# Kernel optimization log

Hardware: AMD Instinct MI355X
Metric: run time of the kernel (lower is better)

## Reference

```python
import jax, jax.numpy as jnp
import numpy as np

D_MODEL = 1024
NUM_HEADS = 16
HEAD_DIM = D_MODEL // NUM_HEADS
HIDDEN = 4096
EPS = 1e-5


def setup_inputs() -> dict:
    key = jax.random.key(0)
    ks = jax.random.split(key, 10)
    s = 0.02
    return {
        "x": jax.random.normal(ks[0], (2, 2048, D_MODEL), dtype=jnp.float32),
        # attention projection weights stored as (in, out): y = x @ W
        "wq": jax.random.normal(ks[1], (D_MODEL, D_MODEL), dtype=jnp.float32) * s,
        "wk": jax.random.normal(ks[2], (D_MODEL, D_MODEL), dtype=jnp.float32) * s,
        "wv": jax.random.normal(ks[3], (D_MODEL, D_MODEL), dtype=jnp.float32) * s,
        "wo": jax.random.normal(ks[4], (D_MODEL, D_MODEL), dtype=jnp.float32) * s,
        # FFN
        "w1": jax.random.normal(ks[5], (D_MODEL, HIDDEN), dtype=jnp.float32) * s,
        "b1": jnp.zeros((HIDDEN,), dtype=jnp.float32),
        "w2": jax.random.normal(ks[6], (HIDDEN, D_MODEL), dtype=jnp.float32) * s,
        "b2": jnp.zeros((D_MODEL,), dtype=jnp.float32),
        # LayerNorms
        "g1": jnp.ones((D_MODEL,), dtype=jnp.float32),
        "be1": jnp.zeros((D_MODEL,), dtype=jnp.float32),
        "g2": jnp.ones((D_MODEL,), dtype=jnp.float32),
        "be2": jnp.zeros((D_MODEL,), dtype=jnp.float32),
    }


def _layernorm(x, g, b):
    mu = jnp.mean(x, axis=-1, keepdims=True)
    var = jnp.mean(jnp.square(x - mu), axis=-1, keepdims=True)
    return (x - mu) * jax.lax.rsqrt(var + EPS) * g + b


def _attention(x, wq, wk, wv, wo):
    B, S, D = x.shape
    q = (x @ wq).reshape(B, S, NUM_HEADS, HEAD_DIM)
    k = (x @ wk).reshape(B, S, NUM_HEADS, HEAD_DIM)
    v = (x @ wv).reshape(B, S, NUM_HEADS, HEAD_DIM)
    scores = jnp.einsum("bqhd,bkhd->bhqk", q, k) / jnp.sqrt(
        jnp.float32(HEAD_DIM)
    )
    causal = jnp.tril(jnp.ones((S, S), dtype=bool))
    scores = jnp.where(causal, scores, -jnp.inf)
    probs = jax.nn.softmax(scores, axis=-1)
    out = jnp.einsum("bhqk,bkhd->bqhd", probs, v).reshape(B, S, D)
    return out @ wo


def _ffn(x, w1, b1, w2, b2):
    return jax.nn.relu(x @ w1 + b1) @ w2 + b2


def reference(x, wq, wk, wv, wo, w1, b1, w2, b2, g1, be1, g2, be2):
    x = x + _attention(_layernorm(x, g1, be1), wq, wk, wv, wo)
    x = x + _ffn(_layernorm(x, g2, be2), w1, b1, w2, b2)
    return x
```

## Files before the change

kernel.cpp:

```cpp
#include <hip/hip_runtime.h>
#include <stdint.h>

typedef unsigned short bf16u;
typedef __attribute__((ext_vector_type(8))) __bf16 bf16x8;
typedef __attribute__((ext_vector_type(4))) float f32x4;
typedef __attribute__((ext_vector_type(4))) unsigned short u16x4;

typedef __attribute__((address_space(1))) void gvoid_t;
typedef __attribute__((address_space(3))) void lvoid_t;

#define SEQ 2048
#define DM 1024

__device__ __forceinline__ bf16u f2bf(float f) {
  union { float f; uint32_t u; } v; v.f = f;
  uint32_t u = v.u + 0x7fffu + ((v.u >> 16) & 1u);
  return (bf16u)(u >> 16);
}

__device__ __forceinline__ void async_copy16(const bf16u* g, const bf16u* l) {
  __builtin_amdgcn_global_load_lds((gvoid_t*)(uintptr_t)g,
                                   (lvoid_t*)(uint32_t)(uintptr_t)l,
                                   16, 0, 0);
}

__global__ __launch_bounds__(256) void ln_kernel(const float* __restrict__ x,
                                                 const float* __restrict__ g,
                                                 const float* __restrict__ be,
                                                 bf16u* __restrict__ out) {
  const int row = blockIdx.x;
  const int t = threadIdx.x;
  const float4 v = ((const float4*)(x + (size_t)row * DM))[t];
  float s  = v.x + v.y + v.z + v.w;
  float ss = v.x * v.x + v.y * v.y + v.z * v.z + v.w * v.w;
#pragma unroll
  for (int m = 1; m < 64; m <<= 1) {
    s  += __shfl_xor(s, m, 64);
    ss += __shfl_xor(ss, m, 64);
  }
  __shared__ float red[2][4];
  const int wv = t >> 6, ln = t & 63;
  if (ln == 0) { red[0][wv] = s; red[1][wv] = ss; }
  __syncthreads();
  s  = red[0][0] + red[0][1] + red[0][2] + red[0][3];
  ss = red[1][0] + red[1][1] + red[1][2] + red[1][3];
  const float mu = s * (1.0f / DM);
  const float var = ss * (1.0f / DM) - mu * mu;
  const float rstd = rsqrtf(var + 1e-5f);
  const float4 gg = ((const float4*)g)[t];
  const float4 bb = ((const float4*)be)[t];
  u16x4 o;
  o[0] = f2bf((v.x - mu) * rstd * gg.x + bb.x);
  o[1] = f2bf((v.y - mu) * rstd * gg.y + bb.y);
  o[2] = f2bf((v.z - mu) * rstd * gg.z + bb.z);
  o[3] = f2bf((v.w - mu) * rstd * gg.w + bb.w);
  *(u16x4*)(out + (size_t)row * DM + t * 4) = o;
}

__global__ __launch_bounds__(256) void wtrans(const float* __restrict__ in,
                                              bf16u* __restrict__ out, int R, int C) {
  __shared__ float tile[32][33];
  const int c0 = blockIdx.x * 32, r0 = blockIdx.y * 32;
  const int tx = threadIdx.x, ty = threadIdx.y;
#pragma unroll
  for (int i = 0; i < 4; ++i)
    tile[ty + i * 8][tx] = in[(size_t)(r0 + ty + i * 8) * C + c0 + tx];
  __syncthreads();
#pragma unroll
  for (int i = 0; i < 4; ++i)
    out[(size_t)(c0 + ty + i * 8) * R + r0 + tx] = f2bf(tile[tx][ty + i * 8]);
}

__global__ __launch_bounds__(256) void wtrans4(const float* __restrict__ a,
                                               const float* __restrict__ b,
                                               const float* __restrict__ c,
                                               const float* __restrict__ d,
                                               bf16u* __restrict__ out) {
  const float* srcs[4] = {a, b, c, d};
  const float* in = srcs[blockIdx.z];
  bf16u* o = out + (size_t)blockIdx.z * 1024 * 1024;
  __shared__ float tile[32][33];
  const int c0 = blockIdx.x * 32, r0 = blockIdx.y * 32;
  const int tx = threadIdx.x, ty = threadIdx.y;
#pragma unroll
  for (int i = 0; i < 4; ++i)
    tile[ty + i * 8][tx] = in[(size_t)(r0 + ty + i * 8) * 1024 + c0 + tx];
  __syncthreads();
#pragma unroll
  for (int i = 0; i < 4; ++i)
    o[(size_t)(c0 + ty + i * 8) * 1024 + r0 + tx] = f2bf(tile[tx][ty + i * 8]);
}

__global__ __launch_bounds__(256) void vtrans(const bf16u* __restrict__ qkv,
                                              bf16u* __restrict__ vt) {
  __shared__ bf16u tile[32][33];
  const int s0 = blockIdx.x * 32;
  const int d0 = blockIdx.y * 32;
  const int bh = blockIdx.z, b = bh >> 4, h = bh & 15;
  const int tx = threadIdx.x, ty = threadIdx.y;
#pragma unroll
  for (int i = 0; i < 4; ++i)
    tile[ty + i * 8][tx] =
        qkv[(size_t)(b * SEQ + s0 + ty + i * 8) * 3072 + 2048 + h * 64 + d0 + tx];
  __syncthreads();
#pragma unroll
  for (int i = 0; i < 4; ++i)
    vt[(size_t)(bh * 64 + d0 + ty + i * 8) * SEQ + s0 + tx] = tile[tx][ty + i * 8];
}

#define VM_WAIT(n) asm volatile("s_waitcnt vmcnt(" #n ")" ::: "memory")
#define BARRIER()  asm volatile("s_barrier" ::: "memory")

__global__ __launch_bounds__(256, 3) void gemm_bt(
    const bf16u* __restrict__ A, const bf16u* __restrict__ Bt,
    int M, int N, int K,
    const float* __restrict__ bias, const float* __restrict__ resid,
    bf16u* __restrict__ outB, float* __restrict__ outF, int mode) {
  __shared__ bf16u As0[128 * 32], As1[128 * 32];
  __shared__ bf16u Bs0[128 * 32], Bs1[128 * 32];
  const int t = threadIdx.x;
  const int wv = t >> 6, ln = t & 63;
  const int col16 = ln & 15, quad = ln >> 4;
  const int wm = wv & 1, wn = wv >> 1;
  const int m0 = blockIdx.y * 128, n0 = blockIdx.x * 128;

  const int c0 = t, c1 = 256 + t;
  const bf16u* ga0 = A + (size_t)(m0 + (c0 >> 2)) * K + (c0 & 3) * 8;
  const bf16u* ga1 = A + (size_t)(m0 + (c1 >> 2)) * K + (c1 & 3) * 8;
  const bf16u* gb0 = Bt + (size_t)(n0 + (c0 >> 2)) * K + (c0 & 3) * 8;
  const bf16u* gb1 = Bt + (size_t)(n0 + (c1 >> 2)) * K + (c1 & 3) * 8;

  const int aoff = (wm * 64 + col16) * 32 + quad * 8;
  const int boff = (wn * 64 + col16) * 32 + quad * 8;

  f32x4 acc[4][4] = {};

  auto stage = [&](bf16u* dA, bf16u* dB) {
    async_copy16(ga0, dA + (size_t)c0 * 8);
    async_copy16(ga1, dA + (size_t)c1 * 8);
    async_copy16(gb0, dB + (size_t)c0 * 8);
    async_copy16(gb1, dB + (size_t)c1 * 8);
    ga0 += 32; ga1 += 32; gb0 += 32; gb1 += 32;
  };
  auto compute = [&](const bf16u* sA, const bf16u* sB) {
    bf16x8 af[4], bfv[4];
#pragma unroll
    for (int i = 0; i < 4; ++i) af[i] = *(const bf16x8*)(sA + aoff + i * 512);
#pragma unroll
    for (int i = 0; i < 4; ++i) bfv[i] = *(const bf16x8*)(sB + boff + i * 512);
#pragma unroll
    for (int mi = 0; mi < 4; ++mi)
#pragma unroll
      for (int ni = 0; ni < 4; ++ni)
        acc[mi][ni] = __builtin_amdgcn_mfma_f32_16x16x32_bf16(af[mi], bfv[ni],
                                                              acc[mi][ni], 0, 0, 0);
  };

  const int niter = K >> 5;
  stage(As0, Bs0);
  for (int k = 0; k < niter; k += 2) {
    stage(As1, Bs1);
    VM_WAIT(4);
    BARRIER();
    compute(As0, Bs0);
    BARRIER();
    if (k + 2 < niter) {
      stage(As0, Bs0);
      VM_WAIT(4);
    } else {
      VM_WAIT(0);
    }
    BARRIER();
    compute(As1, Bs1);
    BARRIER();
  }

#pragma unroll
  for (int mi = 0; mi < 4; ++mi) {
#pragma unroll
    for (int ni = 0; ni < 4; ++ni) {
      const int col = n0 + wn * 64 + ni * 16 + col16;
#pragma unroll
      for (int r = 0; r < 4; ++r) {
        const int row = m0 + wm * 64 + mi * 16 + quad * 4 + r;
        float v = acc[mi][ni][r];
        if (mode == 1 || mode == 3) v += bias[col];
        if (mode == 1) v = fmaxf(v, 0.0f);
        if (mode >= 2) {
          outF[(size_t)row * N + col] = v + resid[(size_t)row * N + col];
        } else {
          outB[(size_t)row * N + col] = f2bf(v);
        }
      }
    }
  }
}

__global__ __launch_bounds__(256, 3) void gemm_bt64(
    const bf16u* __restrict__ A, const bf16u* __restrict__ Bt,
    int M, int N, int K,
    const float* __restrict__ bias, const float* __restrict__ resid,
    bf16u* __restrict__ outB, float* __restrict__ outF, int mode) {
  __shared__ bf16u As0[64 * 64], As1[64 * 64];
  __shared__ bf16u Bs0[128 * 64], Bs1[128 * 64];
  const int t = threadIdx.x;
  const int ln = t & 63;
  const int wv = t >> 6;
  const int col16 = ln & 15, quad = ln >> 4;
  const int m0 = blockIdx.y * 64, n0 = blockIdx.x * 128;

  const bf16u* gA[2];
  const bf16u* gB[4];
#pragma unroll
  for (int j = 0; j < 2; ++j) {
    const int c = t + 256 * j, row = c >> 3, slot = (c & 7) ^ (row & 7);
    gA[j] = A + (size_t)(m0 + row) * K + slot * 8;
  }
#pragma unroll
  for (int j = 0; j < 4; ++j) {
    const int c = t + 256 * j, row = c >> 3, slot = (c & 7) ^ (row & 7);
    gB[j] = Bt + (size_t)(n0 + row) * K + slot * 8;
  }

  f32x4 acc[4][2] = {};

  auto stage = [&](bf16u* dA, bf16u* dB) {
#pragma unroll
    for (int j = 0; j < 2; ++j) {
      async_copy16(gA[j], dA + (size_t)(t + 256 * j) * 8);
      gA[j] += 64;
    }
#pragma unroll
    for (int j = 0; j < 4; ++j) {
      async_copy16(gB[j], dB + (size_t)(t + 256 * j) * 8);
      gB[j] += 64;
    }
  };
  auto compute = [&](const bf16u* sA, const bf16u* sB) {
    bf16x8 af[4][2], bfv[2][2];
#pragma unroll
    for (int mi = 0; mi < 4; ++mi) {
      const int row = mi * 16 + col16;
#pragma unroll
      for (int kc = 0; kc < 2; ++kc)
        af[mi][kc] = *(const bf16x8*)(sA + row * 64 + (((kc << 2) + quad) ^ (row & 7)) * 8);
    }
#pragma unroll
    for (int ni = 0; ni < 2; ++ni) {
      const int row = wv * 32 + ni * 16 + col16;
#pragma unroll
      for (int kc = 0; kc < 2; ++kc)
        bfv[ni][kc] = *(const bf16x8*)(sB + row * 64 + (((kc << 2) + quad) ^ (row & 7)) * 8);
    }
#pragma unroll
    for (int kc = 0; kc < 2; ++kc)
#pragma unroll
      for (int mi = 0; mi < 4; ++mi)
#pragma unroll
        for (int ni = 0; ni < 2; ++ni)
          acc[mi][ni] = __builtin_amdgcn_mfma_f32_16x16x32_bf16(af[mi][kc], bfv[ni][kc],
                                                                acc[mi][ni], 0, 0, 0);
  };

  const int niter = K >> 6;
  stage(As0, Bs0);
  for (int k = 0; k < niter; k += 2) {
    stage(As1, Bs1);
    VM_WAIT(6);
    BARRIER();
    compute(As0, Bs0);
    BARRIER();
    if (k + 2 < niter) {
      stage(As0, Bs0);
      VM_WAIT(6);
    } else {
      VM_WAIT(0);
    }
    BARRIER();
    compute(As1, Bs1);
    BARRIER();
  }

#pragma unroll
  for (int mi = 0; mi < 4; ++mi) {
#pragma unroll
    for (int ni = 0; ni < 2; ++ni) {
      const int col = n0 + wv * 32 + ni * 16 + col16;
#pragma unroll
      for (int r = 0; r < 4; ++r) {
        const int row = m0 + mi * 16 + quad * 4 + r;
        float v = acc[mi][ni][r];
        if (mode == 1 || mode == 3) v += bias[col];
        if (mode == 1) v = fmaxf(v, 0.0f);
        if (mode >= 2) {
          outF[(size_t)row * N + col] = v + resid[(size_t)row * N + col];
        } else {
          outB[(size_t)row * N + col] = f2bf(v);
        }
      }
    }
  }
}

#define PST 132
#define SCL 0.18033688f
__global__ __launch_bounds__(256, 3) void attn_kernel(const bf16u* __restrict__ qkv,
                                                      const bf16u* __restrict__ vt,
                                                      bf16u* __restrict__ out) {
  __shared__ bf16u Ks[128 * 64];
  __shared__ bf16u Vts[2 * 64 * 64];
  __shared__ bf16u pbuf[4][16 * PST];
  __shared__ float lred[4][16];
  const int t = threadIdx.x;
  const int wv = t >> 6, ln = t & 63;
  const int col = ln & 15, quad = ln >> 4;
  const int bh = blockIdx.x, b = bh >> 4, h = bh & 15;
  const int strip = 31 - blockIdx.y;
  const int q0 = strip * 64;
  const int qw = q0 + wv * 16;
  const int qmax = qw + 15;
  const int ntiles = (q0 >> 7) + 1;

  int krow[4], kslot[4], vrow[4], vsub[4], vslot[4];
  const bf16u *kl[4], *vl[4];
#pragma unroll
  for (int j = 0; j < 4; ++j) {
    const int c = t + 256 * j;
    krow[j] = c >> 3; kslot[j] = (c & 7) ^ (krow[j] & 7);
    const int rem = c & 511;
    vsub[j] = c >> 9; vrow[j] = rem >> 3; vslot[j] = (rem & 7) ^ (vrow[j] & 7);
    kl[j] = Ks + (size_t)c * 8;
    vl[j] = Vts + (size_t)c * 8;
  }

  bf16x8 qf0, qf1;
  {
    const size_t qoff = (size_t)(b * SEQ + qw + col) * 3072 + h * 64 + quad * 8;
    qf0 = *(const bf16x8*)(qkv + qoff);
    qf1 = *(const bf16x8*)(qkv + qoff + 32);
  }
  f32x4 po[4] = {};
  float ll[4] = {};

  for (int kb = 0; kb < ntiles; ++kb) {
    const int kbase = kb * 128;
#pragma unroll
    for (int j = 0; j < 4; ++j) {
      async_copy16(qkv + (size_t)(b * SEQ + kbase + krow[j]) * 3072 + 1024 + h * 64 + kslot[j] * 8, kl[j]);
      async_copy16(vt + (size_t)(bh * 64 + vrow[j]) * SEQ + kbase + vsub[j] * 64 + vslot[j] * 8, vl[j]);
    }
    asm volatile("s_waitcnt vmcnt(0)" ::: "memory");
    __syncthreads();

    if (kb < ntiles - 1) {
      f32x4 sc[8];
#pragma unroll
      for (int n = 0; n < 8; ++n) {
        const int kr = n * 16 + col;
        const bf16x8 k0 = *(const bf16x8*)(Ks + kr * 64 + (quad ^ (kr & 7)) * 8);
        const bf16x8 k1 = *(const bf16x8*)(Ks + kr * 64 + ((4 + quad) ^ (kr & 7)) * 8);
        f32x4 z = {};
        z = __builtin_amdgcn_mfma_f32_16x16x32_bf16(qf0, k0, z, 0, 0, 0);
        sc[n] = __builtin_amdgcn_mfma_f32_16x16x32_bf16(qf1, k1, z, 0, 0, 0);
      }
#pragma unroll
      for (int r = 0; r < 4; ++r) {
#pragma unroll
        for (int n = 0; n < 8; ++n) {
          const float e = exp2f(sc[n][r] * SCL);
          ll[r] += e;
          pbuf[wv][(quad * 4 + r) * PST + n * 16 + col] = f2bf(e);
        }
      }
    } else {
      f32x4 sc[8];
      bool act[8];
#pragma unroll
      for (int n = 0; n < 8; ++n) {
        act[n] = (kbase + n * 16) <= qmax;
        if (act[n]) {
          const int kr = n * 16 + col;
          const bf16x8 k0 = *(const bf16x8*)(Ks + kr * 64 + (quad ^ (kr & 7)) * 8);
          const bf16x8 k1 = *(const bf16x8*)(Ks + kr * 64 + ((4 + quad) ^ (kr & 7)) * 8);
          f32x4 z = {};
          z = __builtin_amdgcn_mfma_f32_16x16x32_bf16(qf0, k0, z, 0, 0, 0);
          sc[n] = __builtin_amdgcn_mfma_f32_16x16x32_bf16(qf1, k1, z, 0, 0, 0);
        }
      }
#pragma unroll
      for (int r = 0; r < 4; ++r) {
        const int q = qw + quad * 4 + r;
#pragma unroll
        for (int n = 0; n < 8; ++n) {
          float e = 0.0f;
          if (act[n]) {
            float v = sc[n][r] * SCL;
            v = (kbase + n * 16 + col <= q) ? v : -1e30f;
            e = exp2f(v);
          }
          ll[r] += e;
          pbuf[wv][(quad * 4 + r) * PST + n * 16 + col] = f2bf(e);
        }
      }
    }
    asm volatile("s_waitcnt lgkmcnt(0)" ::: "memory");
    bf16x8 pa[4];
#pragma unroll
    for (int kc = 0; kc < 4; ++kc)
      pa[kc] = *(const bf16x8*)(&pbuf[wv][col * PST + kc * 32 + quad * 8]);
    if (kb < ntiles - 1) {
#pragma unroll
      for (int n = 0; n < 4; ++n) {
        const int vr = n * 16 + col;
#pragma unroll
        for (int kc = 0; kc < 4; ++kc) {
          const bf16x8 vfr = *(const bf16x8*)(Vts + (kc >> 1) * 4096 + vr * 64 +
                                              (((kc & 1) * 4 + quad) ^ (vr & 7)) * 8);
          po[n] = __builtin_amdgcn_mfma_f32_16x16x32_bf16(vfr, pa[kc], po[n], 0, 0, 0);
        }
      }
    } else {
#pragma unroll
      for (int n = 0; n < 4; ++n) {
        const int vr = n * 16 + col;
#pragma unroll
        for (int kc = 0; kc < 4; ++kc)
          if (kbase + kc * 32 <= qmax) {
            const bf16x8 vfr = *(const bf16x8*)(Vts + (kc >> 1) * 4096 + vr * 64 +
                                                (((kc & 1) * 4 + quad) ^ (vr & 7)) * 8);
            po[n] = __builtin_amdgcn_mfma_f32_16x16x32_bf16(vfr, pa[kc], po[n], 0, 0, 0);
          }
      }
    }
    asm volatile("s_waitcnt lgkmcnt(0)" ::: "memory");
    __syncthreads();
  }

#pragma unroll
  for (int m = 1; m < 16; m <<= 1)
#pragma unroll
    for (int r = 0; r < 4; ++r) ll[r] += __shfl_xor(ll[r], m, 64);
  if (col == 0) {
#pragma unroll
    for (int r = 0; r < 4; ++r) lred[wv][quad * 4 + r] = ll[r];
  }
  asm volatile("s_waitcnt lgkmcnt(0)" ::: "memory");
  const float inv = 1.0f / lred[wv][col];
#pragma unroll
  for (int n = 0; n < 4; ++n) {
    u16x4 o;
#pragma unroll
    for (int r = 0; r < 4; ++r) o[r] = f2bf(po[n][r] * inv);
    *(u16x4*)(out + (size_t)(b * SEQ + qw + col) * DM + h * 64 + n * 16 + quad * 4) = o;
  }
}

extern "C" void kernel_launch(void* const* d_in, const int* in_sizes, int n_in,
                              void* d_out, int out_size, void* d_ws, size_t ws_size,
                              hipStream_t stream) {
  const float* x   = (const float*)d_in[0];
  const float* wq  = (const float*)d_in[1];
  const float* wk  = (const float*)d_in[2];
  const float* wvv = (const float*)d_in[3];
  const float* wo  = (const float*)d_in[4];
  const float* w1  = (const float*)d_in[5];
  const float* b1  = (const float*)d_in[6];
  const float* w2  = (const float*)d_in[7];
  const float* b2  = (const float*)d_in[8];
  const float* g1  = (const float*)d_in[9];
  const float* be1 = (const float*)d_in[10];
  const float* g2  = (const float*)d_in[11];
  const float* be2 = (const float*)d_in[12];
  float* out = (float*)d_out;

  char* ws = (char*)d_ws;
  bf16u* wqkv_t = (bf16u*)(ws);
  bf16u* wo_t   = (bf16u*)(ws +  6291456);
  bf16u* w1_t   = (bf16u*)(ws +  8388608);
  bf16u* w2_t   = (bf16u*)(ws + 16777216);
  bf16u* lnbuf  = (bf16u*)(ws + 25165824);
  bf16u* qkv    = (bf16u*)(ws + 33554432);
  bf16u* vtb    = (bf16u*)(ws + 58720256);
  bf16u* h1     = (bf16u*)(ws + 33554432);
  bf16u* attn   = lnbuf;

  const dim3 tb32(32, 8);
  wtrans4<<<dim3(32, 32, 4), tb32, 0, stream>>>(wq, wk, wvv, wo, wqkv_t);
  wtrans<<<dim3(128, 32), tb32, 0, stream>>>(w1, w1_t, 1024, 4096);
  wtrans<<<dim3(32, 128), tb32, 0, stream>>>(w2, w2_t, 4096, 1024);

  ln_kernel<<<4096, 256, 0, stream>>>(x, g1, be1, lnbuf);
  gemm_bt<<<dim3(24, 32), 256, 0, stream>>>(lnbuf, wqkv_t, 4096, 3072, 1024,
                                            nullptr, nullptr, qkv, nullptr, 0);
  vtrans<<<dim3(64, 2, 32), tb32, 0, stream>>>(qkv, vtb);
  attn_kernel<<<dim3(32, 32), 256, 0, stream>>>(qkv, vtb, attn);
  gemm_bt64<<<dim3(8, 64), 256, 0, stream>>>(attn, wo_t, 4096, 1024, 1024,
                                             nullptr, x, nullptr, out, 2);
  ln_kernel<<<4096, 256, 0, stream>>>(out, g2, be2, lnbuf);
  gemm_bt<<<dim3(32, 32), 256, 0, stream>>>(lnbuf, w1_t, 4096, 4096, 1024,
                                            b1, nullptr, h1, nullptr, 1);
  gemm_bt64<<<dim3(8, 64), 256, 0, stream>>>(h1, w2_t, 4096, 1024, 4096,
                                             b2, out, nullptr, out, 3);
}
```

Before: 355.5 us.

## Replace 128x128 GEMM with 256x256 8-wave pipelined GEMM and XCD-aware block swizzle

Replaces the 128x128-tile, 256-thread bf16 GEMM used for the QKV and FFN1 projections with a 256x256-tile, 512-thread kernel. It uses a 64-wide K step, XOR-swizzled LDS layout, quarter-staged async loads interleaved with MFMA quadrants, and s_setprio around the MFMA blocks. Block indices are remapped so neighbouring tiles land on the same XCD, and the same remap is added to gemm_bt64. The aim is more data reuse per LDS load and better L2 locality. The cost is one workgroup per CU with 128KB LDS and a grid of only 192 or 256 blocks on 256 CUs, so some CUs sit idle for the QKV projection.

```diff
diff --git a/kernel.cpp b/kernel.cpp
--- a/kernel.cpp
+++ b/kernel.cpp
@@ -23,6 +23,10 @@
                                    (lvoid_t*)(uint32_t)(uintptr_t)l,
                                    16, 0, 0);
 }
+
+#define VM_WAIT(n) asm volatile("s_waitcnt vmcnt(" #n ")" ::: "memory")
+#define LGKM0()    asm volatile("s_waitcnt lgkmcnt(0)" ::: "memory")
+#define BARRIER()  asm volatile("s_barrier" ::: "memory")
 
 __global__ __launch_bounds__(256) void ln_kernel(const float* __restrict__ x,
                                                  const float* __restrict__ g,
@@ -108,89 +112,145 @@
     vt[(size_t)(bh * 64 + d0 + ty + i * 8) * SEQ + s0 + tx] = tile[tx][ty + i * 8];
 }
 
-#define VM_WAIT(n) asm volatile("s_waitcnt vmcnt(" #n ")" ::: "memory")
-#define BARRIER()  asm volatile("s_barrier" ::: "memory")
-
-__global__ __launch_bounds__(256, 3) void gemm_bt(
+__global__ __launch_bounds__(512, 1) void gemm256(
     const bf16u* __restrict__ A, const bf16u* __restrict__ Bt,
     int M, int N, int K,
-    const float* __restrict__ bias, const float* __restrict__ resid,
-    bf16u* __restrict__ outB, float* __restrict__ outF, int mode) {
-  __shared__ bf16u As0[128 * 32], As1[128 * 32];
-  __shared__ bf16u Bs0[128 * 32], Bs1[128 * 32];
+    const float* __restrict__ bias, bf16u* __restrict__ outB, int mode) {
+  __shared__ bf16u sh[2][32768];
   const int t = threadIdx.x;
-  const int wv = t >> 6, ln = t & 63;
+  const int ln = t & 63;
+  const int wv = t >> 6;
   const int col16 = ln & 15, quad = ln >> 4;
-  const int wm = wv & 1, wn = wv >> 1;
-  const int m0 = blockIdx.y * 128, n0 = blockIdx.x * 128;
-
-  const int c0 = t, c1 = 256 + t;
-  const bf16u* ga0 = A + (size_t)(m0 + (c0 >> 2)) * K + (c0 & 3) * 8;
-  const bf16u* ga1 = A + (size_t)(m0 + (c1 >> 2)) * K + (c1 & 3) * 8;
-  const bf16u* gb0 = Bt + (size_t)(n0 + (c0 >> 2)) * K + (c0 & 3) * 8;
-  const bf16u* gb1 = Bt + (size_t)(n0 + (c1 >> 2)) * K + (c1 & 3) * 8;
-
-  const int aoff = (wm * 64 + col16) * 32 + quad * 8;
-  const int boff = (wn * 64 + col16) * 32 + quad * 8;
-
-  f32x4 acc[4][4] = {};
-
-  auto stage = [&](bf16u* dA, bf16u* dB) {
-    async_copy16(ga0, dA + (size_t)c0 * 8);
-    async_copy16(ga1, dA + (size_t)c1 * 8);
-    async_copy16(gb0, dB + (size_t)c0 * 8);
-    async_copy16(gb1, dB + (size_t)c1 * 8);
-    ga0 += 32; ga1 += 32; gb0 += 32; gb1 += 32;
+  const int wm = wv >> 2, wn = wv & 3;
+
+  const int nbx = N >> 8;
+  const int nwg = nbx * (M >> 8);
+  const int cpx = nwg >> 3;
+  const int bid = blockIdx.x;
+  const int swz = (bid & 7) * cpx + (bid >> 3);
+  const int m0 = (swz / nbx) << 8, n0 = (swz % nbx) << 8;
+
+  const bf16u* gsrc[4][2];
+  int doff[4][2];
+#pragma unroll
+  for (int j = 0; j < 2; ++j) {
+    const int c = t + (j << 9);
+    const int lr = c >> 3, slot = (c & 7) ^ (lr & 7);
+    const int ra = (lr & 63) + ((lr >> 6) << 7);
+    const int rb = (lr & 31) + ((lr >> 5) << 6);
+    gsrc[0][j] = A  + (size_t)(m0 + ra) * K + slot * 8;
+    gsrc[3][j] = A  + (size_t)(m0 + ra + 64) * K + slot * 8;
+    gsrc[1][j] = Bt + (size_t)(n0 + rb) * K + slot * 8;
+    gsrc[2][j] = Bt + (size_t)(n0 + rb + 32) * K + slot * 8;
+    doff[0][j] = c * 8;
+    doff[3][j] = 8192 + c * 8;
+    doff[1][j] = 16384 + c * 8;
+    doff[2][j] = 24576 + c * 8;
+  }
+
+  const int sx = col16 & 7;
+  int aoffs[4][2], boffs[2][2];
+#pragma unroll
+  for (int i = 0; i < 4; ++i)
+#pragma unroll
+    for (int kc = 0; kc < 2; ++kc)
+      aoffs[i][kc] = (wm * 64 + i * 16 + col16) * 64 + (((kc << 2) + quad) ^ sx) * 8;
+#pragma unroll
+  for (int i = 0; i < 2; ++i)
+#pragma unroll
+    for (int kc = 0; kc < 2; ++kc)
+      boffs[i][kc] = 16384 + (wn * 32 + i * 16 + col16) * 64 + (((kc << 2) + quad) ^ sx) * 8;
+
+  f32x4 acc[8][4] = {};
+  bf16x8 Af[4][2], Bf[4][2];
+
+  auto stage = [&](int s, int b) {
+#pragma unroll
+    for (int j = 0; j < 2; ++j) {
+      async_copy16(gsrc[s][j], &sh[b][doff[s][j]]);
+      gsrc[s][j] += 64;
+    }
   };
-  auto compute = [&](const bf16u* sA, const bf16u* sB) {
-    bf16x8 af[4], bfv[4];
-#pragma unroll
-    for (int i = 0; i < 4; ++i) af[i] = *(const bf16x8*)(sA + aoff + i * 512);
-#pragma unroll
-    for (int i = 0; i < 4; ++i) bfv[i] = *(const bf16x8*)(sB + boff + i * 512);
-#pragma unroll
-    for (int mi = 0; mi < 4; ++mi)
-#pragma unroll
-      for (int ni = 0; ni < 4; ++ni)
-        acc[mi][ni] = __builtin_amdgcn_mfma_f32_16x16x32_bf16(af[mi], bfv[ni],
-                                                              acc[mi][ni], 0, 0, 0);
+  auto readA = [&](int b, int mh) {
+#pragma unroll
+    for (int i = 0; i < 4; ++i)
+#pragma unroll
+      for (int kc = 0; kc < 2; ++kc)
+        Af[i][kc] = *(const bf16x8*)(&sh[b][mh * 8192 + aoffs[i][kc]]);
   };
-
-  const int niter = K >> 5;
-  stage(As0, Bs0);
-  for (int k = 0; k < niter; k += 2) {
-    stage(As1, Bs1);
-    VM_WAIT(4);
+  auto readB = [&](int b, int nh) {
+#pragma unroll
+    for (int i = 0; i < 2; ++i)
+#pragma unroll
+      for (int kc = 0; kc < 2; ++kc)
+        Bf[nh * 2 + i][kc] = *(const bf16x8*)(&sh[b][nh * 8192 + boffs[i][kc]]);
+  };
+  auto mfmaQ = [&](int mh, int nh) {
+#pragma unroll
+    for (int kc = 0; kc < 2; ++kc)
+#pragma unroll
+      for (int mi = 0; mi < 4; ++mi)
+#pragma unroll
+        for (int nl = 0; nl < 2; ++nl)
+          acc[mh * 4 + mi][nh * 2 + nl] = __builtin_amdgcn_mfma_f32_16x16x32_bf16(
+              Af[mi][kc], Bf[nh * 2 + nl][kc], acc[mh * 4 + mi][nh * 2 + nl], 0, 0, 0);
+  };
+
+  const int nt = K >> 6;
+  stage(0, 0); stage(1, 0); stage(2, 0); stage(3, 0);
+  VM_WAIT(4);
+  BARRIER();
+
+  int bsel = 0;
+  for (int kt = 0; kt < nt - 1; ++kt, bsel ^= 1) {
+    const int bn = bsel ^ 1;
+    readA(bsel, 0); readB(bsel, 0);
+    stage(0, bn);
+    BARRIER(); LGKM0();
+    __builtin_amdgcn_s_setprio(1); mfmaQ(0, 0); __builtin_amdgcn_s_setprio(0);
+    VM_WAIT(4); BARRIER();
+    readB(bsel, 1);
+    stage(1, bn);
+    BARRIER(); LGKM0();
+    __builtin_amdgcn_s_setprio(1); mfmaQ(0, 1); __builtin_amdgcn_s_setprio(0);
+    VM_WAIT(4); BARRIER();
+    readA(bsel, 1);
+    stage(2, bn);
+    BARRIER(); LGKM0();
+    __builtin_amdgcn_s_setprio(1); mfmaQ(1, 0); __builtin_amdgcn_s_setprio(0);
     BARRIER();
-    compute(As0, Bs0);
-    BARRIER();
-    if (k + 2 < niter) {
-      stage(As0, Bs0);
-      VM_WAIT(4);
-    } else {
-      VM_WAIT(0);
-    }
-    BARRIER();
-    compute(As1, Bs1);
-    BARRIER();
-  }
-
-#pragma unroll
-  for (int mi = 0; mi < 4; ++mi) {
-#pragma unroll
-    for (int ni = 0; ni < 4; ++ni) {
-      const int col = n0 + wn * 64 + ni * 16 + col16;
+    stage(3, bn);
+    __builtin_amdgcn_s_setprio(1); mfmaQ(1, 1); __builtin_amdgcn_s_setprio(0);
+    VM_WAIT(4); BARRIER();
+  }
+  readA(bsel, 0); readB(bsel, 0);
+  BARRIER(); LGKM0();
+  __builtin_amdgcn_s_setprio(1); mfmaQ(0, 0); __builtin_amdgcn_s_setprio(0);
+  VM_WAIT(2); BARRIER();
+  readB(bsel, 1);
+  BARRIER(); LGKM0();
+  __builtin_amdgcn_s_setprio(1); mfmaQ(0, 1); __builtin_amdgcn_s_setprio(0);
+  VM_WAIT(0); BARRIER();
+  readA(bsel, 1);
+  LGKM0();
+  __builtin_amdgcn_s_setprio(1); mfmaQ(1, 0); mfmaQ(1, 1); __builtin_amdgcn_s_setprio(0);
+
+  float bv[4];
+  if (mode == 1) {
+#pragma unroll
+    for (int n = 0; n < 4; ++n) bv[n] = bias[n0 + wn * 64 + n * 16 + col16];
+  }
+#pragma unroll
+  for (int mi = 0; mi < 8; ++mi) {
+#pragma unroll
+    for (int n = 0; n < 4; ++n) {
+      const int col = n0 + wn * 64 + n * 16 + col16;
 #pragma unroll
       for (int r = 0; r < 4; ++r) {
-        const int row = m0 + wm * 64 + mi * 16 + quad * 4 + r;
-        float v = acc[mi][ni][r];
-        if (mode == 1 || mode == 3) v += bias[col];
-        if (mode == 1) v = fmaxf(v, 0.0f);
-        if (mode >= 2) {
-          outF[(size_t)row * N + col] = v + resid[(size_t)row * N + col];
-        } else {
-          outB[(size_t)row * N + col] = f2bf(v);
-        }
+        const int row = m0 + wm * 128 + mi * 16 + quad * 4 + r;
+        float v = acc[mi][n][r];
+        if (mode == 1) v = fmaxf(v + bv[n], 0.0f);
+        outB[(size_t)row * N + col] = f2bf(v);
       }
     }
   }
@@ -207,7 +267,13 @@
   const int ln = t & 63;
   const int wv = t >> 6;
   const int col16 = ln & 15, quad = ln >> 4;
-  const int m0 = blockIdx.y * 64, n0 = blockIdx.x * 128;
+
+  const int nbx = gridDim.x;
+  const int nwg = nbx * gridDim.y;
+  const int cpx = nwg >> 3;
+  const int flat = blockIdx.y * nbx + blockIdx.x;
+  const int swz = (flat & 7) * cpx + (flat >> 3);
+  const int m0 = (swz / nbx) * 64, n0 = (swz % nbx) * 128;
 
   const bf16u* gA[2];
   const bf16u* gB[4];
@@ -490,15 +556,15 @@
   wtrans<<<dim3(32, 128), tb32, 0, stream>>>(w2, w2_t, 4096, 1024);
 
   ln_kernel<<<4096, 256, 0, stream>>>(x, g1, be1, lnbuf);
-  gemm_bt<<<dim3(24, 32), 256, 0, stream>>>(lnbuf, wqkv_t, 4096, 3072, 1024,
-                                            nullptr, nullptr, qkv, nullptr, 0);
+  gemm256<<<192, 512, 0, stream>>>(lnbuf, wqkv_t, 4096, 3072, 1024,
+                                   nullptr, qkv, 0);
   vtrans<<<dim3(64, 2, 32), tb32, 0, stream>>>(qkv, vtb);
   attn_kernel<<<dim3(32, 32), 256, 0, stream>>>(qkv, vtb, attn);
   gemm_bt64<<<dim3(8, 64), 256, 0, stream>>>(attn, wo_t, 4096, 1024, 1024,
                                              nullptr, x, nullptr, out, 2);
   ln_kernel<<<4096, 256, 0, stream>>>(out, g2, be2, lnbuf);
-  gemm_bt<<<dim3(32, 32), 256, 0, stream>>>(lnbuf, w1_t, 4096, 4096, 1024,
-                                            b1, nullptr, h1, nullptr, 1);
+  gemm256<<<256, 512, 0, stream>>>(lnbuf, w1_t, 4096, 4096, 1024,
+                                   b1, h1, 1);
   gemm_bt64<<<dim3(8, 64), 256, 0, stream>>>(h1, w2_t, 4096, 1024, 4096,
                                              b2, out, nullptr, out, 3);
 }
```

After: 329.2 us. -7.4%, faster.
